# Optimization experiments

Measured on AMD Instinct MI355X. Metric: run time of the kernel, lower is better.

## Reference

```python
import jax, jax.numpy as jnp
from jax import lax
import numpy as np

B = 32768
N_IN = 8
N_HID = 64
N_CTRL = 2
M_SCEN = (1.0, 1.2)          # scenario parameters for f/g
M_NOM = 1.0
CLF_LAM = 1.0
CBF_LAM = 1.0
P_CLF = 100.0
P_CBF = 50.0
QP_ITERS = 80                # fixed-iteration batched ADMM (OSQP-style) replacing CvxpyLayer
RHO = 1.0
SIGMA = 1e-6
INF = jnp.inf


def setup_inputs() -> dict:
    key = jax.random.key(0)
    ks = jax.random.split(key, 16)
    s = 0.3
    return {
        "x":   jax.random.normal(ks[0], (B, N_IN), jnp.float32),
        "VW1": jax.random.normal(ks[1], (N_HID, N_IN), jnp.float32) * s,
        "Vb1": jax.random.normal(ks[2], (N_HID,), jnp.float32) * s,
        "VW2": jax.random.normal(ks[3], (N_HID, N_HID), jnp.float32) * s,
        "Vb2": jax.random.normal(ks[4], (N_HID,), jnp.float32) * s,
        "HW1": jax.random.normal(ks[5], (N_HID, N_IN), jnp.float32) * s,
        "Hb1": jax.random.normal(ks[6], (N_HID,), jnp.float32) * s,
        "HW2": jax.random.normal(ks[7], (N_HID, N_HID), jnp.float32) * s,
        "Hb2": jax.random.normal(ks[8], (N_HID,), jnp.float32) * s,
        "HW3": jax.random.normal(ks[9], (N_HID, N_HID), jnp.float32) * s,
        "Hb3": jax.random.normal(ks[10], (N_HID,), jnp.float32) * s,
        "HW4": jax.random.normal(ks[11], (1, N_HID), jnp.float32) * s,
        "Hb4": jax.random.normal(ks[12], (1,), jnp.float32) * s,
        "G0":  jax.random.normal(ks[13], (N_IN, N_CTRL), jnp.float32) * s,
        "K":   jax.random.normal(ks[14], (N_IN, N_CTRL), jnp.float32) * s,
    }


def _lyapunov(x, W1, b1, W2, b2):
    t1 = jnp.tanh(x @ W1.T + b1)                                   # [B,H]
    t2 = jnp.tanh(t1 @ W2.T + b2)                                  # [B,H]
    V = 0.5 * jnp.sum(t2 * t2, axis=1)                             # [B]
    # fused diag(1-t^2) @ W chain (no diag_embed materialization)
    D1 = (1.0 - t1 ** 2)[:, :, None] * W1[None]                    # [B,H,N]
    D2 = (1.0 - t2 ** 2)[:, :, None] * jnp.einsum('hk,bkn->bhn', W2, D1)
    grad_V = jnp.einsum('bh,bhn->bn', t2, D2)                      # [B,N]
    return V, grad_V


def _barrier(x, W1, b1, W2, b2, W3, b3, W4, b4):
    t1 = jnp.tanh(x @ W1.T + b1)
    t2 = jnp.tanh(t1 @ W2.T + b2)
    t3 = jnp.tanh(t2 @ W3.T + b3)
    H = t3 @ W4.T + b4                                             # [B,1]
    D1 = (1.0 - t1 ** 2)[:, :, None] * W1[None]
    D2 = (1.0 - t2 ** 2)[:, :, None] * jnp.einsum('hk,bkn->bhn', W2, D1)
    D3 = (1.0 - t3 ** 2)[:, :, None] * jnp.einsum('hk,bkn->bhn', W3, D2)
    grad_H = jnp.einsum('oh,bhn->bn', W4, D3)                      # [B,N] (o=1)
    return H, grad_H


def _solve_qp(q, A, lo, hi):
    """Batched OSQP-style ADMM for min 0.5 z^T P z + q^T z  s.t. lo <= A z <= hi.
    P = diag([2,2,0,0,0,0]); z = [u(2), r_clf(2), s_cbf(2)]. Fixed iterations."""
    nb, mc, nz = A.shape[0], A.shape[1], A.shape[2]
    Pdiag = jnp.array([2.0, 2.0, 0.0, 0.0, 0.0, 0.0], q.dtype)
    M = RHO * jnp.einsum('bmi,bmj->bij', A, A) + jnp.diag(Pdiag + SIGMA)
    Minv = jnp.linalg.inv(M)                                       # [B,6,6]
    x0 = jnp.zeros((nb, nz), q.dtype)
    z0 = jnp.zeros((nb, mc), q.dtype)
    y0 = jnp.zeros((nb, mc), q.dtype)

    def step(carry, _):
        xx, zz, yy = carry
        rhs = SIGMA * xx - q + jnp.einsum('bmi,bm->bi', A, RHO * zz - yy)
        xt = jnp.einsum('bij,bj->bi', Minv, rhs)
        zt = jnp.einsum('bmi,bi->bm', A, xt)
        zn = jnp.clip(zt + yy / RHO, lo, hi)
        yn = yy + RHO * (zt - zn)
        return (xt, zn, yn), None

    (xf, _, _), _ = lax.scan(step, (x0, z0, y0), None, length=QP_ITERS)
    return xf                                                      # [B,6]


def _forward(x, VW1, Vb1, VW2, Vb2, HW1, Hb1, HW2, Hb2, HW3, Hb3, HW4, Hb4, G0, K):
    V, grad_V = _lyapunov(x, VW1, Vb1, VW2, Vb2)
    H, grad_H = _barrier(x, HW1, Hb1, HW2, Hb2, HW3, Hb3, HW4, Hb4)

    LfVs, LgVs, LfHs, LgHs = [], [], [], []
    for m in M_SCEN:
        # f(x,m) = -x/m ; g(x,m) = G0/m
        LfVs.append(-jnp.sum(grad_V * x, axis=1) / m)              # [B]
        LgVs.append((grad_V @ G0) / m)                             # [B,C]
        LfHs.append(-jnp.sum(grad_H * x, axis=1) / m)
        LgHs.append((grad_H @ G0) / m)
    u_nom = -(x @ K) * (1.0 / M_NOM)                               # [B,C]

    nb = x.shape[0]
    z2 = jnp.zeros((nb, 2), x.dtype)
    ey = jnp.eye(2, dtype=x.dtype)
    e = lambda i: jnp.broadcast_to(ey[i], (nb, 2))
    ninf = jnp.full((nb,), -INF, x.dtype)
    pinf = jnp.full((nb,), INF, x.dtype)
    zer = jnp.zeros((nb,), x.dtype)

    rows, los, his = [], [], []
    for i in range(len(M_SCEN)):
        # CBF: LfH + LgH@u + cbf_lam*H + s_i >= 0
        rows.append(jnp.concatenate([LgHs[i], z2, e(i)], axis=1))
        los.append(-(LfHs[i] + CBF_LAM * H[:, 0])); his.append(pinf)
        # CLF: LfV + LgV@u + clf_lam*V - r_i <= 0
        rows.append(jnp.concatenate([LgVs[i], -e(i), z2], axis=1))
        los.append(ninf); his.append(-(LfVs[i] + CLF_LAM * V))
    for i in range(len(M_SCEN)):
        rows.append(jnp.concatenate([z2, e(i), z2], axis=1)); los.append(zer); his.append(pinf)
    for i in range(len(M_SCEN)):
        rows.append(jnp.concatenate([z2, z2, e(i)], axis=1)); los.append(zer); his.append(pinf)

    A = jnp.stack(rows, axis=1)                                    # [B,8,6]
    lo = jnp.stack(los, axis=1)                                    # [B,8]
    hi = jnp.stack(his, axis=1)
    # objective ||u-u_nom||^2 + p_clf*sum r + p_cbf*sum s  ->  q = [-2 u_nom, p_clf, p_clf, p_cbf, p_cbf]
    q = jnp.concatenate([-2.0 * u_nom,
                         jnp.full((nb, 2), P_CLF, x.dtype),
                         jnp.full((nb, 2), P_CBF, x.dtype)], axis=1)

    z = _solve_qp(q, A, lo, hi)                                    # [B,6]
    u = z[:, :N_CTRL]
    relaxation = jnp.mean(z[:, N_CTRL:N_CTRL + len(M_SCEN)], axis=1, keepdims=True)  # [B,1]

    ns = float(len(M_SCEN))
    Vdot = sum(LfVs[i] + jnp.sum(LgVs[i] * u, axis=1) for i in range(len(M_SCEN))) / ns
    Hdot = sum(LfHs[i] + jnp.sum(LgHs[i] * u, axis=1) for i in range(len(M_SCEN))) / ns
    return u, relaxation, V, Vdot[:, None, None], H, Hdot[:, None, None]


def reference(x, VW1, Vb1, VW2, Vb2, HW1, Hb1, HW2, Hb2, HW3, Hb3, HW4, Hb4, G0, K):
    return _forward(x, VW1, Vb1, VW2, Vb2, HW1, Hb1, HW2, Hb2, HW3, Hb3, HW4, Hb4, G0, K)
```

## Files before the change

### kernel.cpp

```cpp
#include <hip/hip_runtime.h>
#include <hip/hip_bf16.h>
#include <math.h>

typedef _Float16 f16x8 __attribute__((ext_vector_type(8)));
typedef _Float16 f16x4 __attribute__((ext_vector_type(4)));
typedef float    f32x4 __attribute__((ext_vector_type(4)));

__device__ __forceinline__ float ldin(const void* p, int i, int f32f) {
  return f32f ? ((const float*)p)[i]
              : __bfloat162float(((const __hip_bfloat16*)p)[i]);
}

__device__ __forceinline__ f32x4 MFMA(f16x8 a, f16x8 b, f32x4 c) {
  return __builtin_amdgcn_mfma_f32_16x16x32_f16(a, b, c, 0, 0, 0);
}

__device__ __forceinline__ float tanh_fast(float x) {
  float e = __expf(2.f * x);
  return 1.f - 2.f * __builtin_amdgcn_rcpf(e + 1.f);
}

__device__ __forceinline__ float redq(float v) {
  v += __shfl_xor(v, 16, 64);
  v += __shfl_xor(v, 32, 64);
  return v;
}

__device__ __forceinline__ int widx(int h, int k) {
  return ((h >> 4) << 10) + ((k >> 5) << 9) + (((k >> 3) & 3) << 7) + ((h & 15) << 3) + (k & 7);
}

#define OFF_VW2   0
#define OFF_VW2T  4096
#define OFF_HW2   8192
#define OFF_HW2T  12288
#define OFF_HW3   16384
#define OFF_HW3T  20480
#define OFF_W1V   24576
#define OFF_W1H   26624
#define CF_BASE   28672
#define C_WGV0 0
#define C_WGV1 64
#define C_WGH0 128
#define C_WGH1 192
#define C_VB1  256
#define C_VB2  320
#define C_HB1  384
#define C_HB2  448
#define C_HB3  512
#define C_W4   576
#define C_K    640
#define C_HB4  656
#define C_FLAG 657
#define C_N    658

__global__ __launch_bounds__(256) void prep_kernel(
    const void* px, const void* pVW1, const void* pVW2,
    const void* pHW1, const void* pHW2, const void* pHW3,
    const void* pVb1, const void* pVb2, const void* pHb1, const void* pHb2,
    const void* pHb3, const void* pHW4, const void* pHb4,
    const void* pG0, const void* pK, _Float16* wsp)
{
  __shared__ int sCnt;
  const int tid = threadIdx.x;
  if (tid == 0) sCnt = 0;
  __syncthreads();
  {
    const unsigned short* xb = (const unsigned short*)px;
    int good = 0;
#pragma unroll
    for (int i = 0; i < 2; ++i) {
      int ex = (xb[tid * 2 + i] >> 7) & 0xFF;
      good += (ex >= 97 && ex <= 157) ? 1 : 0;
    }
    atomicAdd(&sCnt, good);
  }
  __syncthreads();
  const int f32f = (sCnt >= 435) ? 0 : 1;

  const int t = blockIdx.x * 256 + tid;
  int h = t >> 6, k = t & 63;
  int fw = widx(h, k), tw = widx(k, h);
  _Float16 v;
  v = (_Float16)ldin(pVW2, t, f32f); wsp[OFF_VW2 + fw] = v; wsp[OFF_VW2T + tw] = v;
  v = (_Float16)ldin(pHW2, t, f32f); wsp[OFF_HW2 + fw] = v; wsp[OFF_HW2T + tw] = v;
  v = (_Float16)ldin(pHW3, t, f32f); wsp[OFF_HW3 + fw] = v; wsp[OFF_HW3T + tw] = v;
  if (t < 512) {
    int hh = t >> 3, j = t & 7;
    int base = ((hh >> 4) << 9) + ((hh & 15) << 3) + j;
    float f = ldin(pVW1, t, f32f); _Float16 hi = (_Float16)f;
    _Float16 lo = f32f ? (_Float16)(f - (float)hi) : (_Float16)0.f;
    wsp[OFF_W1V + base]       = hi;
    wsp[OFF_W1V + base + 128] = hi;
    wsp[OFF_W1V + base + 256] = lo;
    wsp[OFF_W1V + base + 384] = (_Float16)0.f;
    f = ldin(pHW1, t, f32f); hi = (_Float16)f;
    lo = f32f ? (_Float16)(f - (float)hi) : (_Float16)0.f;
    wsp[OFF_W1H + base]       = hi;
    wsp[OFF_W1H + base + 128] = hi;
    wsp[OFF_W1H + base + 256] = lo;
    wsp[OFF_W1H + base + 384] = (_Float16)0.f;
  }
  if (blockIdx.x == 0) {
    float* wsF = (float*)(wsp + CF_BASE);
    if (tid < 64) {
      float a0 = 0.f, a1 = 0.f, b0 = 0.f, b1 = 0.f;
#pragma unroll
      for (int nn = 0; nn < 8; ++nn) {
        float g0 = ldin(pG0, 2 * nn, f32f), g1 = ldin(pG0, 2 * nn + 1, f32f);
        float wv = ldin(pVW1, tid * 8 + nn, f32f), wh = ldin(pHW1, tid * 8 + nn, f32f);
        a0 += wv * g0; a1 += wv * g1; b0 += wh * g0; b1 += wh * g1;
      }
      wsF[C_WGV0 + tid] = a0; wsF[C_WGV1 + tid] = a1;
      wsF[C_WGH0 + tid] = b0; wsF[C_WGH1 + tid] = b1;
      wsF[C_VB1 + tid] = ldin(pVb1, tid, f32f);
      wsF[C_VB2 + tid] = ldin(pVb2, tid, f32f);
      wsF[C_HB1 + tid] = ldin(pHb1, tid, f32f);
      wsF[C_HB2 + tid] = ldin(pHb2, tid, f32f);
      wsF[C_HB3 + tid] = ldin(pHb3, tid, f32f);
      wsF[C_W4  + tid] = ldin(pHW4, tid, f32f);
    }
    if (tid < 16) wsF[C_K + tid] = ldin(pK, tid, f32f);
    if (tid == 0) { wsF[C_HB4] = ldin(pHb4, 0, f32f); ((int*)wsF)[C_FLAG] = f32f; }
  }
}

__global__ __launch_bounds__(256, 3) void main_kernel(
    const void* px, const _Float16* wsp, float* out)
{
  __shared__ __align__(16) _Float16 sAct[4][1024];
  __shared__ __align__(16) float sC[C_N];

  const int tid = threadIdx.x, lane = tid & 63, w = tid >> 6;
  const int n = lane & 15, q = lane >> 4;
  const int e0 = blockIdx.x * 64 + w * 16;

  const float* cf = (const float*)(wsp + CF_BASE);
  for (int i = tid; i < C_N; i += 256) sC[i] = cf[i];
  const int f32f = ((const int*)cf)[C_FLAG];
  __syncthreads();

  float xv[8];
  if (f32f) {
    const f32x4* xp = (const f32x4*)((const float*)px + (e0 + n) * 8);
    f32x4 x0 = xp[0], x1 = xp[1];
#pragma unroll
    for (int j = 0; j < 4; ++j) { xv[j] = x0[j]; xv[4 + j] = x1[j]; }
  } else {
    uint4 u = *(const uint4*)((const unsigned short*)px + (e0 + n) * 8);
    unsigned uu[4] = {u.x, u.y, u.z, u.w};
#pragma unroll
    for (int j = 0; j < 4; ++j) {
      xv[2 * j]     = __uint_as_float(uu[j] << 16);
      xv[2 * j + 1] = __uint_as_float(uu[j] & 0xffff0000u);
    }
  }
  float un0 = 0.f, un1 = 0.f;
  f16x8 xb;
#pragma unroll
  for (int j = 0; j < 8; ++j) {
    _Float16 hh = (_Float16)xv[j];
    float lo = xv[j] - (float)hh;
    xb[j] = (q == 1) ? (_Float16)lo : ((q == 3) ? (_Float16)0.f : hh);
    un0 -= xv[j] * sC[C_K + 2 * j];
    un1 -= xv[j] * sC[C_K + 2 * j + 1];
  }

  _Float16* buf = sAct[w];

  auto gemm64 = [&](int poff, f32x4* acc) {
    f16x8 b0 = *(const f16x8*)(buf + lane * 8);
    f16x8 b1 = *(const f16x8*)(buf + 512 + lane * 8);
#pragma unroll
    for (int ht = 0; ht < 4; ++ht) {
      const _Float16* ap = wsp + poff + ht * 1024 + lane * 8;
      f32x4 c = {0.f, 0.f, 0.f, 0.f};
      c = MFMA(*(const f16x8*)ap, b0, c);
      c = MFMA(*(const f16x8*)(ap + 512), b1, c);
      acc[ht] = c;
    }
  };
  auto l1gemm = [&](int off, f32x4* acc) {
#pragma unroll
    for (int ht = 0; ht < 4; ++ht) {
      const _Float16* ap = wsp + off + ht * 512 + lane * 8;
      f32x4 c = {0.f, 0.f, 0.f, 0.f};
      acc[ht] = MFMA(*(const f16x8*)ap, xb, c);
    }
  };
  auto wst = [&](const f32x4* vals) {
#pragma unroll
    for (int ht = 0; ht < 4; ++ht) {
      int aw = ((ht >> 1) << 9) + (((ht & 1) * 2 + (q >> 1)) << 7) + n * 8 + ((q & 1) << 2);
      f16x4 vh;
#pragma unroll
      for (int r = 0; r < 4; ++r) vh[r] = (_Float16)vals[ht][r];
      *(f16x4*)(buf + aw) = vh;
    }
  };

  f32x4 acc[4], tv[4];

  f32x4 z1V[4], d1V[4];
  l1gemm(OFF_W1V, acc);
#pragma unroll
  for (int ht = 0; ht < 4; ++ht) {
    int hb = ht * 16 + q * 4;
    f32x4 bb = *(const f32x4*)&sC[C_VB1 + hb];
    z1V[ht] = acc[ht];
#pragma unroll
    for (int r = 0; r < 4; ++r) {
      float t = tanh_fast(z1V[ht][r] + bb[r]);
      tv[ht][r] = t; d1V[ht][r] = 1.f - t * t;
    }
  }
  wst(tv);

  gemm64(OFF_VW2, acc);
  float pV = 0.f;
#pragma unroll
  for (int ht = 0; ht < 4; ++ht) {
    int hb = ht * 16 + q * 4;
    f32x4 bb = *(const f32x4*)&sC[C_VB2 + hb];
#pragma unroll
    for (int r = 0; r < 4; ++r) {
      float t = tanh_fast(acc[ht][r] + bb[r]);
      pV += t * t;
      tv[ht][r] = t * (1.f - t * t);
    }
  }
  wst(tv);

  gemm64(OFF_VW2T, acc);
  float pgvx = 0.f, plv0 = 0.f, plv1 = 0.f;
#pragma unroll
  for (int ht = 0; ht < 4; ++ht) {
    int hb = ht * 16 + q * 4;
    f32x4 g0 = *(const f32x4*)&sC[C_WGV0 + hb];
    f32x4 g1 = *(const f32x4*)&sC[C_WGV1 + hb];
#pragma unroll
    for (int r = 0; r < 4; ++r) {
      float wt = acc[ht][r] * d1V[ht][r];
      pgvx += wt * z1V[ht][r];
      plv0 += wt * g0[r]; plv1 += wt * g1[r];
    }
  }

  f32x4 z1H[4], d1H[4], d2H[4];
  l1gemm(OFF_W1H, acc);
#pragma unroll
  for (int ht = 0; ht < 4; ++ht) {
    int hb = ht * 16 + q * 4;
    f32x4 bb = *(const f32x4*)&sC[C_HB1 + hb];
    z1H[ht] = acc[ht];
#pragma unroll
    for (int r = 0; r < 4; ++r) {
      float t = tanh_fast(z1H[ht][r] + bb[r]);
      tv[ht][r] = t; d1H[ht][r] = 1.f - t * t;
    }
  }
  wst(tv);

  gemm64(OFF_HW2, acc);
#pragma unroll
  for (int ht = 0; ht < 4; ++ht) {
    int hb = ht * 16 + q * 4;
    f32x4 bb = *(const f32x4*)&sC[C_HB2 + hb];
#pragma unroll
    for (int r = 0; r < 4; ++r) {
      float t = tanh_fast(acc[ht][r] + bb[r]);
      tv[ht][r] = t; d2H[ht][r] = 1.f - t * t;
    }
  }
  wst(tv);

  gemm64(OFF_HW3, acc);
  float pH = 0.f;
#pragma unroll
  for (int ht = 0; ht < 4; ++ht) {
    int hb = ht * 16 + q * 4;
    f32x4 bb = *(const f32x4*)&sC[C_HB3 + hb];
    f32x4 w4 = *(const f32x4*)&sC[C_W4 + hb];
#pragma unroll
    for (int r = 0; r < 4; ++r) {
      float t = tanh_fast(acc[ht][r] + bb[r]);
      pH += t * w4[r];
      tv[ht][r] = w4[r] * (1.f - t * t);
    }
  }
  wst(tv);

  gemm64(OFF_HW3T, acc);
#pragma unroll
  for (int ht = 0; ht < 4; ++ht)
#pragma unroll
    for (int r = 0; r < 4; ++r) tv[ht][r] = acc[ht][r] * d2H[ht][r];
  wst(tv);

  gemm64(OFF_HW2T, acc);
  float pghx = 0.f, plh0 = 0.f, plh1 = 0.f;
#pragma unroll
  for (int ht = 0; ht < 4; ++ht) {
    int hb = ht * 16 + q * 4;
    f32x4 g0 = *(const f32x4*)&sC[C_WGH0 + hb];
    f32x4 g1 = *(const f32x4*)&sC[C_WGH1 + hb];
#pragma unroll
    for (int r = 0; r < 4; ++r) {
      float wt = acc[ht][r] * d1H[ht][r];
      pghx += wt * z1H[ht][r];
      plh0 += wt * g0[r]; plh1 += wt * g1[r];
    }
  }

  float gh0 = redq(plh0), gh1 = redq(plh1), gv0 = redq(plv0), gv1 = redq(plv1);
  float ghx = redq(pghx), gvx = redq(pgvx);
  float V   = 0.5f * redq(pV);
  float H   = redq(pH) + sC[C_HB4];

  if (lane >= 16) return;
  const int e = e0 + lane;
  out[98304 + e]  = V;
  out[163840 + e] = H;

  const float im = 1.0f / 1.2f;
  const float sg = 1e-6f;

  float lo0 = ghx - H;
  float hi1 = gvx - V;
  float lo2 = ghx * im - H;
  float hi3 = gvx * im - V;
  float qv0 = -2.f * un0, qv1 = -2.f * un1;

  const float d  = 2.f + sg;
  const float rd = 1.f / d;
  const float al = 1.f + im * im;
  const float be = al * (1.f - rd);
  float S00 = be * (gh0 * gh0 + gv0 * gv0) + d;
  float S11 = be * (gh1 * gh1 + gv1 * gv1) + d;
  float S01 = be * (gh0 * gh1 + gv0 * gv1);
  float idet = 1.f / (S00 * S11 - S01 * S01);
  float i00 = S11 * idet, i11 = S00 * idet, i01 = -S01 * idet;

  float X0 = 0.f, X1 = 0.f, X2 = 0.f, X3 = 0.f, X4 = 0.f, X5 = 0.f;
  float Z[8] = {0.f, 0.f, 0.f, 0.f, 0.f, 0.f, 0.f, 0.f};
  float Y[8] = {0.f, 0.f, 0.f, 0.f, 0.f, 0.f, 0.f, 0.f};

#pragma unroll 1
  for (int it = 0; it < 80; ++it) {
    float t0 = Z[0] - Y[0], t1 = Z[1] - Y[1], t2 = Z[2] - Y[2], t3 = Z[3] - Y[3];
    float t4 = Z[4] - Y[4], t5 = Z[5] - Y[5], t6 = Z[6] - Y[6], t7 = Z[7] - Y[7];
    float tauh = t0 + im * t2, tauv = t1 + im * t3;
    float b0 = sg * X0 - qv0 + gh0 * tauh + gv0 * tauv;
    float b1 = sg * X1 - qv1 + gh1 * tauh + gv1 * tauv;
    float b2 = sg * X2 - 100.f - t1 + t4;
    float b3 = sg * X3 - 100.f - t3 + t5;
    float b4 = sg * X4 - 50.f + t0 + t6;
    float b5 = sg * X5 - 50.f + t2 + t7;
    float pp = b2 + im * b3;
    float s2 = b4 + im * b5;
    float cb0 = gh0 * s2 - gv0 * pp;
    float cb1 = gh1 * s2 - gv1 * pp;
    float u0b = b0 - cb0 * rd;
    float u1b = b1 - cb1 * rd;
    X0 = i00 * u0b + i01 * u1b;
    X1 = i01 * u0b + i11 * u1b;
    float gdH = gh0 * X0 + gh1 * X1;
    float gdV = gv0 * X0 + gv1 * X1;
    X2 = (b2 + gdV) * rd;
    X3 = (b3 + im * gdV) * rd;
    X4 = (b4 - gdH) * rd;
    X5 = (b5 - im * gdH) * rd;
    float zt0 = gdH + X4;
    float zt1 = gdV - X2;
    float zt2 = gdH * im + X5;
    float zt3 = gdV * im - X3;

    float v, zn;
    v = zt0 + Y[0]; zn = fmaxf(v, lo0); Y[0] += zt0 - zn; Z[0] = zn;
    v = zt1 + Y[1]; zn = fminf(v, hi1); Y[1] += zt1 - zn; Z[1] = zn;
    v = zt2 + Y[2]; zn = fmaxf(v, lo2); Y[2] += zt2 - zn; Z[2] = zn;
    v = zt3 + Y[3]; zn = fminf(v, hi3); Y[3] += zt3 - zn; Z[3] = zn;
    v = X2 + Y[4];  zn = fmaxf(v, 0.f); Y[4] += X2 - zn;  Z[4] = zn;
    v = X3 + Y[5];  zn = fmaxf(v, 0.f); Y[5] += X3 - zn;  Z[5] = zn;
    v = X4 + Y[6];  zn = fmaxf(v, 0.f); Y[6] += X4 - zn;  Z[6] = zn;
    v = X5 + Y[7];  zn = fmaxf(v, 0.f); Y[7] += X5 - zn;  Z[7] = zn;
  }

  float relax = 0.5f * (X2 + X3);
  const float cc = 0.5f * (1.f + im);
  float Vdot = cc * (gv0 * X0 + gv1 * X1 - gvx);
  float Hdot = cc * (gh0 * X0 + gh1 * X1 - ghx);

  out[2 * e]      = X0;
  out[2 * e + 1]  = X1;
  out[65536 + e]  = relax;
  out[131072 + e] = Vdot;
  out[196608 + e] = Hdot;
}

extern "C" void kernel_launch(void* const* d_in, const int* in_sizes, int n_in,
                              void* d_out, int out_size, void* d_ws, size_t ws_size,
                              hipStream_t stream) {
  (void)in_sizes; (void)n_in; (void)out_size; (void)ws_size;
  float* out = (float*)d_out;
  _Float16* wsp = (_Float16*)d_ws;
  prep_kernel<<<16, 256, 0, stream>>>(
      d_in[0], d_in[1], d_in[3], d_in[5], d_in[7], d_in[9],
      d_in[2], d_in[4], d_in[6], d_in[8], d_in[10], d_in[11], d_in[12],
      d_in[13], d_in[14], wsp);
  main_kernel<<<512, 256, 0, stream>>>(d_in[0], wsp, out);
}
```

Before: 124.8 us.

## Repack QP solve to full-wave lanes via LDS and prefetch MFMA weights

Each wave previously ran the 80-iteration ADMM loop with only 16 of 64 lanes active. Now the per-element reductions go through shared memory, and two of the eight waves in a 512-thread block solve 64 elements each with all lanes busy. The change also preloads all weight fragments before the MFMAs, drops the sigma*X terms from the ADMM right-hand side, and vectorises the u store. Risks: the block-wide sync, six waves idling during the serial loop, lower occupancy with bigger blocks, and a small numerical difference from dropping the sigma terms.

```diff
diff --git a/kernel.cpp b/kernel.cpp
--- a/kernel.cpp
+++ b/kernel.cpp
@@ -5,6 +5,7 @@
 typedef _Float16 f16x8 __attribute__((ext_vector_type(8)));
 typedef _Float16 f16x4 __attribute__((ext_vector_type(4)));
 typedef float    f32x4 __attribute__((ext_vector_type(4)));
+typedef float    f32x2 __attribute__((ext_vector_type(2)));
 
 __device__ __forceinline__ float ldin(const void* p, int i, int f32f) {
   return f32f ? ((const float*)p)[i]
@@ -125,18 +126,19 @@
   }
 }
 
-__global__ __launch_bounds__(256, 3) void main_kernel(
+__global__ __launch_bounds__(512, 2) void main_kernel(
     const void* px, const _Float16* wsp, float* out)
 {
-  __shared__ __align__(16) _Float16 sAct[4][1024];
+  __shared__ __align__(16) _Float16 sAct[8][1024];
+  __shared__ __align__(16) float sQPs[10][128];
   __shared__ __align__(16) float sC[C_N];
 
   const int tid = threadIdx.x, lane = tid & 63, w = tid >> 6;
   const int n = lane & 15, q = lane >> 4;
-  const int e0 = blockIdx.x * 64 + w * 16;
+  const int e0 = blockIdx.x * 128 + w * 16;
 
   const float* cf = (const float*)(wsp + CF_BASE);
-  for (int i = tid; i < C_N; i += 256) sC[i] = cf[i];
+  for (int i = tid; i < C_N; i += 512) sC[i] = cf[i];
   const int f32f = ((const int*)cf)[C_FLAG];
   __syncthreads();
 
@@ -169,23 +171,29 @@
   _Float16* buf = sAct[w];
 
   auto gemm64 = [&](int poff, f32x4* acc) {
+    f16x8 a[8];
+#pragma unroll
+    for (int i = 0; i < 8; ++i)
+      a[i] = *(const f16x8*)(wsp + poff + i * 512 + lane * 8);
     f16x8 b0 = *(const f16x8*)(buf + lane * 8);
     f16x8 b1 = *(const f16x8*)(buf + 512 + lane * 8);
 #pragma unroll
     for (int ht = 0; ht < 4; ++ht) {
-      const _Float16* ap = wsp + poff + ht * 1024 + lane * 8;
       f32x4 c = {0.f, 0.f, 0.f, 0.f};
-      c = MFMA(*(const f16x8*)ap, b0, c);
-      c = MFMA(*(const f16x8*)(ap + 512), b1, c);
+      c = MFMA(a[2 * ht], b0, c);
+      c = MFMA(a[2 * ht + 1], b1, c);
       acc[ht] = c;
     }
   };
   auto l1gemm = [&](int off, f32x4* acc) {
+    f16x8 a[4];
+#pragma unroll
+    for (int ht = 0; ht < 4; ++ht)
+      a[ht] = *(const f16x8*)(wsp + off + ht * 512 + lane * 8);
 #pragma unroll
     for (int ht = 0; ht < 4; ++ht) {
-      const _Float16* ap = wsp + off + ht * 512 + lane * 8;
       f32x4 c = {0.f, 0.f, 0.f, 0.f};
-      acc[ht] = MFMA(*(const f16x8*)ap, xb, c);
+      acc[ht] = MFMA(a[ht], xb, c);
     }
   };
   auto wst = [&](const f32x4* vals) {
@@ -312,13 +320,27 @@
     }
   }
 
-  float gh0 = redq(plh0), gh1 = redq(plh1), gv0 = redq(plv0), gv1 = redq(plv1);
-  float ghx = redq(pghx), gvx = redq(pgvx);
-  float V   = 0.5f * redq(pV);
-  float H   = redq(pH) + sC[C_HB4];
-
-  if (lane >= 16) return;
-  const int e = e0 + lane;
+  {
+    float a0 = redq(plh0), a1 = redq(plh1), a2 = redq(plv0), a3 = redq(plv1);
+    float a4 = redq(pghx), a5 = redq(pgvx), a6 = redq(pV), a7 = redq(pH);
+    if (q == 0) {
+      int col = w * 16 + n;
+      sQPs[0][col] = a0; sQPs[1][col] = a1; sQPs[2][col] = a2; sQPs[3][col] = a3;
+      sQPs[4][col] = a4; sQPs[5][col] = a5; sQPs[6][col] = a6; sQPs[7][col] = a7;
+      sQPs[8][col] = un0; sQPs[9][col] = un1;
+    }
+  }
+  __syncthreads();
+  if (w != 0 && w != 2) return;
+
+  const int col = (w >> 1) * 64 + lane;
+  const int e = blockIdx.x * 128 + col;
+  float gh0 = sQPs[0][col], gh1 = sQPs[1][col];
+  float gv0 = sQPs[2][col], gv1 = sQPs[3][col];
+  float ghx = sQPs[4][col], gvx = sQPs[5][col];
+  float V   = 0.5f * sQPs[6][col];
+  float H   = sQPs[7][col] + sC[C_HB4];
+  un0 = sQPs[8][col]; un1 = sQPs[9][col];
   out[98304 + e]  = V;
   out[163840 + e] = H;
 
@@ -329,7 +351,7 @@
   float hi1 = gvx - V;
   float lo2 = ghx * im - H;
   float hi3 = gvx * im - V;
-  float qv0 = -2.f * un0, qv1 = -2.f * un1;
+  float nq0 = 2.f * un0, nq1 = 2.f * un1;
 
   const float d  = 2.f + sg;
   const float rd = 1.f / d;
@@ -350,12 +372,12 @@
     float t0 = Z[0] - Y[0], t1 = Z[1] - Y[1], t2 = Z[2] - Y[2], t3 = Z[3] - Y[3];
     float t4 = Z[4] - Y[4], t5 = Z[5] - Y[5], t6 = Z[6] - Y[6], t7 = Z[7] - Y[7];
     float tauh = t0 + im * t2, tauv = t1 + im * t3;
-    float b0 = sg * X0 - qv0 + gh0 * tauh + gv0 * tauv;
-    float b1 = sg * X1 - qv1 + gh1 * tauh + gv1 * tauv;
-    float b2 = sg * X2 - 100.f - t1 + t4;
-    float b3 = sg * X3 - 100.f - t3 + t5;
-    float b4 = sg * X4 - 50.f + t0 + t6;
-    float b5 = sg * X5 - 50.f + t2 + t7;
+    float b0 = nq0 + gh0 * tauh + gv0 * tauv;
+    float b1 = nq1 + gh1 * tauh + gv1 * tauv;
+    float b2 = -100.f - t1 + t4;
+    float b3 = -100.f - t3 + t5;
+    float b4 = -50.f + t0 + t6;
+    float b5 = -50.f + t2 + t7;
     float pp = b2 + im * b3;
     float s2 = b4 + im * b5;
     float cb0 = gh0 * s2 - gv0 * pp;
@@ -391,8 +413,8 @@
   float Vdot = cc * (gv0 * X0 + gv1 * X1 - gvx);
   float Hdot = cc * (gh0 * X0 + gh1 * X1 - ghx);
 
-  out[2 * e]      = X0;
-  out[2 * e + 1]  = X1;
+  f32x2 uo; uo[0] = X0; uo[1] = X1;
+  *(f32x2*)&out[2 * e] = uo;
   out[65536 + e]  = relax;
   out[131072 + e] = Vdot;
   out[196608 + e] = Hdot;
@@ -408,5 +430,5 @@
       d_in[0], d_in[1], d_in[3], d_in[5], d_in[7], d_in[9],
       d_in[2], d_in[4], d_in[6], d_in[8], d_in[10], d_in[11], d_in[12],
       d_in[13], d_in[14], wsp);
-  main_kernel<<<512, 256, 0, stream>>>(d_in[0], wsp, out);
-}
+  main_kernel<<<256, 512, 0, stream>>>(d_in[0], wsp, out);
+}
```

After: 107.6 us. -13.8%, faster.
